# Kernel optimization log

Measured on AMD Instinct MI355X. Metric: run time of the kernel, lower is better.

Reference implementation:

```python
import jax, jax.numpy as jnp
import numpy as np

N_NODES = 50000
D_IN = 128
HIDDEN = 128
UNITS_DENSE = 256
N_EDGES = 600000
N_PRED = 200000
N_SEL = 300000


def setup_inputs() -> dict:
    key = jax.random.key(0)
    ks = jax.random.split(key, 12)
    node_state = jax.random.normal(ks[0], (N_NODES, D_IN), jnp.float32)
    edge_index = jax.random.randint(ks[1], (2, N_EDGES), 0, N_NODES, jnp.int32)
    out_edges = jax.random.randint(ks[2], (2, N_PRED), 0, N_NODES, jnp.int32)
    set_idx = jnp.sort(jax.random.randint(ks[3], (N_SEL,), 0, 2 * N_PRED, jnp.int32))
    # Glorot-ish scaled weights
    W1 = jax.random.normal(ks[4], (D_IN, HIDDEN), jnp.float32) / np.float32(np.sqrt(D_IN))
    b1 = jnp.zeros((HIDDEN,), jnp.float32)
    W2 = jax.random.normal(ks[5], (HIDDEN, HIDDEN), jnp.float32) / np.float32(np.sqrt(HIDDEN))
    b2 = jnp.zeros((HIDDEN,), jnp.float32)
    dense_W = jax.random.normal(ks[6], (2 * 0 + HIDDEN, UNITS_DENSE), jnp.float32) / np.float32(np.sqrt(HIDDEN))
    dense_b = jnp.zeros((UNITS_DENSE,), jnp.float32)
    out_W = jax.random.normal(ks[7], (UNITS_DENSE, 2), jnp.float32) / np.float32(np.sqrt(UNITS_DENSE))
    out_b = jnp.zeros((2,), jnp.float32)
    return {
        "node_state": node_state, "edge_index": edge_index, "out_edges": out_edges,
        "set_idx": set_idx, "W1": W1, "b1": b1, "W2": W2, "b2": b2,
        "dense_W": dense_W, "dense_b": dense_b, "out_W": out_W, "out_b": out_b,
    }


def _graph_conv(h, src, dst, W, b):
    """DGL GraphConv, norm='both', no activation: D_in^{-1/2} A D_out^{-1/2} H W + b."""
    n = h.shape[0]
    ones = jnp.ones(src.shape[0], h.dtype)
    deg_out = jnp.clip(jax.ops.segment_sum(ones, src, num_segments=n), 1.0)  # [N]
    deg_in = jnp.clip(jax.ops.segment_sum(ones, dst, num_segments=n), 1.0)   # [N]
    h = (h * jax.lax.rsqrt(deg_out)[:, None]) @ W                            # [N, H]
    agg = jax.ops.segment_sum(h[src], dst, num_segments=n)                   # [N, H]
    return agg * jax.lax.rsqrt(deg_in)[:, None] + b


def reference(node_state, edge_index, out_edges, set_idx,
              W1, b1, W2, b2, dense_W, dense_b, out_W, out_b):
    src, dst = edge_index[0], edge_index[1]
    h = _graph_conv(node_state, src, dst, W1, b1)
    h = _graph_conv(h, src, dst, W2, b2)
    # concat along axis=0 as in the original: [2*E_pred, H]
    edge_state = jnp.concatenate([h[out_edges[0]], h[out_edges[1]]], axis=0)
    # boolean_mask replaced by equivalent gather of selected (True) rows
    edge_state_set = edge_state[set_idx]                                      # [N_SEL, H]
    hidden = jax.nn.relu(edge_state_set @ dense_W + dense_b)
    return jax.nn.softmax(hidden @ out_W + out_b, axis=-1)
```

## Files before the change

kernel.cpp:

```cpp
#include <hip/hip_runtime.h>

#define NN 50000
#define DD 128
#define NE 600000
#define NP 200000
#define NS 300000
#define NU 256
#define NBH 128
#define EPB 4688
#define NW 12500
#define NB64 782
#define NSCAN 49

typedef __attribute__((ext_vector_type(8))) short short8;
typedef __attribute__((ext_vector_type(4))) float floatx4;

__device__ inline float bf2f(unsigned int u16) {
    unsigned int x = u16 << 16;
    float f; __builtin_memcpy(&f, &x, 4); return f;
}
__device__ inline unsigned short f2bf(float f) {
    unsigned int x; __builtin_memcpy(&x, &f, 4);
    unsigned int lsb = (x >> 16) & 1u;
    x += 0x7fffu + lsb;
    return (unsigned short)(x >> 16);
}

__global__ __launch_bounds__(256) void k_hist(const int* __restrict__ ei,
                                              unsigned int* __restrict__ P,
                                              unsigned long long* __restrict__ status) {
    __shared__ unsigned int hw[NW];
    int b = blockIdx.x, half = blockIdx.y, tid = threadIdx.x;
    if (b == 0 && half == 0 && tid < 64) status[tid] = 0ull;
    for (int w = tid; w < NW; w += 256) hw[w] = 0;
    __syncthreads();
    const int* src = ei + (size_t)half * NE;
    int e0 = b * EPB, e1 = min(e0 + EPB, NE);
    for (int e = e0 + tid; e < e1; e += 256) {
        int s = src[e];
        atomicAdd(&hw[s >> 2], 1u << ((s & 3) * 8));
    }
    __syncthreads();
    unsigned int* Pb = P + ((size_t)half * NBH + b) * NW;
    for (int w = tid; w < NW; w += 256) Pb[w] = hw[w];
}

__global__ __launch_bounds__(256) void k_mid(
    const unsigned int* __restrict__ P_hist, float* __restrict__ r,
    const float* __restrict__ W1, const float* __restrict__ W2, const float* __restrict__ dW,
    unsigned short* __restrict__ BT1, unsigned short* __restrict__ BT2,
    unsigned short* __restrict__ BTd,
    int* __restrict__ row_ptr, unsigned char* __restrict__ baseb,
    unsigned long long* __restrict__ status)
{
    int b = blockIdx.x, tid = threadIdx.x, lane = tid & 63, w = tid >> 6;
    int gid = b * 256 + tid;

    int4 v = {0, 0, 0, 0};
    if (gid < NW) {
        const unsigned int* Ph = P_hist + (size_t)NBH * NW + gid;
        int c0 = 0, c1 = 0, c2 = 0, c3 = 0;
        for (int b2 = 0; b2 < NBH; ++b2) {
            unsigned int x = Ph[(size_t)b2 * NW];
            c0 += x & 0xff; c1 += (x >> 8) & 0xff; c2 += (x >> 16) & 0xff; c3 += x >> 24;
        }
        v = (int4){c0, c1, c2, c3};
        float4 rr = {rsqrtf((float)max(c0, 1)), rsqrtf((float)max(c1, 1)),
                     rsqrtf((float)max(c2, 1)), rsqrtf((float)max(c3, 1))};
        *(float4*)(r + NN + gid * 4) = rr;
    } else if (gid < 2 * NW) {
        int wl = gid - NW;
        const unsigned int* Ph = P_hist + wl;
        int c0 = 0, c1 = 0, c2 = 0, c3 = 0;
        for (int b2 = 0; b2 < NBH; ++b2) {
            unsigned int x = Ph[(size_t)b2 * NW];
            c0 += x & 0xff; c1 += (x >> 8) & 0xff; c2 += (x >> 16) & 0xff; c3 += x >> 24;
        }
        float4 rr = {rsqrtf((float)max(c0, 1)), rsqrtf((float)max(c1, 1)),
                     rsqrtf((float)max(c2, 1)), rsqrtf((float)max(c3, 1))};
        *(float4*)(r + wl * 4) = rr;
    }

    {
        int t = gid;
        if (t < 16384) { int rr = t >> 7, cc = t & 127; BT1[cc * 128 + rr] = f2bf(W1[t]); }
        else if (t < 32768) { int t2 = t - 16384; int rr = t2 >> 7, cc = t2 & 127; BT2[cc * 128 + rr] = f2bf(W2[t2]); }
        else if (t < 65536) { int t2 = t - 32768; int rr = t2 >> 8, cc = t2 & 255; BTd[cc * 128 + rr] = f2bf(dW[t2]); }
    }

    if (b < NSCAN) {
        __shared__ int wsum[4];
        __shared__ long long sbase;
        int tot = v.x + v.y + v.z + v.w;
        int x = tot;
#pragma unroll
        for (int off = 1; off < 64; off <<= 1) {
            int y = __shfl_up(x, off);
            if (lane >= off) x += y;
        }
        if (lane == 63) wsum[w] = x;
        __syncthreads();
        int woff = 0;
#pragma unroll
        for (int i = 0; i < 4; ++i) if (i < w) woff += wsum[i];
        if (tid == 0) {
            int btot = wsum[0] + wsum[1] + wsum[2] + wsum[3];
            if (b == 0) {
                sbase = 0;
                __threadfence();
                atomicExch(&status[0], (2ull << 62) | (unsigned long long)btot);
            } else {
                __threadfence();
                atomicExch(&status[b], (1ull << 62) | (unsigned long long)btot);
                long long run = 0; int j = b - 1;
                while (true) {
                    unsigned long long s;
                    do { s = atomicAdd(&status[j], 0ull); } while (s == 0ull);
                    run += (long long)(s & 0x3fffffffffffffffull);
                    if ((s >> 62) == 2ull) break;
                    --j;
                }
                sbase = run;
                __threadfence();
                atomicExch(&status[b], (2ull << 62) | (unsigned long long)(run + btot));
            }
        }
        __syncthreads();
        if (gid < NW) {
            int base = (int)sbase + woff + (x - tot);
            int4 o = {base, base + v.x, base + v.x + v.y, base + v.x + v.y + v.z};
            *(int4*)(row_ptr + gid * 4) = o;
        }
        if (b == 0 && tid == 0) row_ptr[NN] = NE;
    }

    int cb = b - NSCAN;
    if (cb >= 0 && cb < 196) {
        int n = cb * 256 + tid;
        if (n < NN) {
            int wl = n >> 2, sh = (n & 3) * 8;
            int run = 0;
            const unsigned int* Pd = P_hist + (size_t)NBH * NW;
            for (int b2 = 0; b2 < NBH; ++b2) {
                baseb[(size_t)b2 * NN + n] = (unsigned char)run;
                run += (Pd[(size_t)b2 * NW + wl] >> sh) & 0xff;
            }
        }
    }
}

__global__ __launch_bounds__(256) void k_gemm1_bucket(
    const float* __restrict__ A, const float* __restrict__ rs,
    const unsigned short* __restrict__ BT, unsigned short* __restrict__ Cm,
    const int* __restrict__ ei, const int* __restrict__ row_ptr,
    const unsigned char* __restrict__ baseb, int* __restrict__ col)
{
    __shared__ unsigned short sm[26112];
    int b = blockIdx.x, tid = threadIdx.x;

    if (b < NBH) {
        unsigned int* cw = (unsigned int*)sm;
        for (int w = tid; w < NW; w += 256) cw[w] = 0;
        __syncthreads();
        const unsigned char* bt = baseb + (size_t)b * NN;
        int e0 = b * EPB, e1 = min(e0 + EPB, NE);
        for (int e = e0 + tid; e < e1; e += 256) {
            int s = ei[e], d = ei[NE + e];
            int sh = (d & 3) * 8;
            unsigned int old = atomicAdd(&cw[d >> 2], 1u << sh);
            col[row_ptr[d] + (int)bt[d] + ((old >> sh) & 0xff)] = s;
        }
        return;
    }

    unsigned short (*As)[136] = (unsigned short(*)[136])sm;
    unsigned short (*Bs)[136] = (unsigned short(*)[136])(sm + 64 * 136);
    int lane = tid & 63, wave = tid >> 6;
    int quad = lane >> 4, l16 = lane & 15;
    int row0 = (b - NBH) * 64;

#pragma unroll
    for (int p = 0; p < 8; ++p) {
        int fid = tid + p * 256;
        int r = fid >> 5, c = fid & 31;
        int gr = row0 + r; if (gr > NN - 1) gr = NN - 1;
        float4 v = *(const float4*)(A + (size_t)gr * DD + c * 4);
        ushort4 u;
        u.x = f2bf(v.x); u.y = f2bf(v.y); u.z = f2bf(v.z); u.w = f2bf(v.w);
        *(ushort4*)&As[r][c * 4] = u;
    }
#pragma unroll
    for (int p = 0; p < 8; ++p) {
        int fid = tid + p * 256;
        int r = fid >> 4, c = fid & 15;
        *(uint4*)&Bs[r][c * 8] = *(const uint4*)(BT + (size_t)r * DD + c * 8);
    }
    __syncthreads();

    short8 af[4];
#pragma unroll
    for (int ks = 0; ks < 4; ++ks)
        af[ks] = *(const short8*)&As[wave * 16 + l16][ks * 32 + quad * 8];
    floatx4 acc[8];
#pragma unroll
    for (int nt = 0; nt < 8; ++nt) acc[nt] = (floatx4){0.f, 0.f, 0.f, 0.f};
#pragma unroll
    for (int ks = 0; ks < 4; ++ks) {
#pragma unroll
        for (int nt = 0; nt < 8; ++nt) {
            short8 bf = *(const short8*)&Bs[nt * 16 + l16][ks * 32 + quad * 8];
            acc[nt] = __builtin_amdgcn_mfma_f32_16x16x32_bf16(af[ks], bf, acc[nt], 0, 0, 0);
        }
    }
    int rbase = row0 + wave * 16 + quad * 4;
#pragma unroll
    for (int r = 0; r < 4; ++r) {
        int gr = rbase + r;
        if (gr < NN) {
            float s = rs[gr];
#pragma unroll
            for (int nt = 0; nt < 8; ++nt)
                Cm[(size_t)gr * DD + nt * 16 + l16] = f2bf(acc[nt][r] * s);
        }
    }
}

__global__ __launch_bounds__(256) void k_gemm_bf(const unsigned short* __restrict__ A,
                                                 const float* __restrict__ rs,
                                                 const unsigned short* __restrict__ BT,
                                                 unsigned short* __restrict__ Cm) {
    __shared__ unsigned short As[64][136];
    __shared__ unsigned short Bs[128][136];
    int tid = threadIdx.x, lane = tid & 63, wave = tid >> 6;
    int quad = lane >> 4, l16 = lane & 15;
    int row0 = blockIdx.x * 64;

#pragma unroll
    for (int p = 0; p < 4; ++p) {
        int fid = tid + p * 256;
        int r = fid >> 4, c = fid & 15;
        int gr = row0 + r; if (gr > NN - 1) gr = NN - 1;
        *(uint4*)&As[r][c * 8] = *(const uint4*)(A + (size_t)gr * DD + c * 8);
    }
#pragma unroll
    for (int p = 0; p < 8; ++p) {
        int fid = tid + p * 256;
        int r = fid >> 4, c = fid & 15;
        *(uint4*)&Bs[r][c * 8] = *(const uint4*)(BT + (size_t)r * DD + c * 8);
    }
    __syncthreads();

    short8 af[4];
#pragma unroll
    for (int ks = 0; ks < 4; ++ks)
        af[ks] = *(const short8*)&As[wave * 16 + l16][ks * 32 + quad * 8];
    floatx4 acc[8];
#pragma unroll
    for (int nt = 0; nt < 8; ++nt) acc[nt] = (floatx4){0.f, 0.f, 0.f, 0.f};
#pragma unroll
    for (int ks = 0; ks < 4; ++ks) {
#pragma unroll
        for (int nt = 0; nt < 8; ++nt) {
            short8 bf = *(const short8*)&Bs[nt * 16 + l16][ks * 32 + quad * 8];
            acc[nt] = __builtin_amdgcn_mfma_f32_16x16x32_bf16(af[ks], bf, acc[nt], 0, 0, 0);
        }
    }
    int rbase = row0 + wave * 16 + quad * 4;
#pragma unroll
    for (int r = 0; r < 4; ++r) {
        int gr = rbase + r;
        if (gr < NN) {
            float s = rs[gr];
#pragma unroll
            for (int nt = 0; nt < 8; ++nt)
                Cm[(size_t)gr * DD + nt * 16 + l16] = f2bf(acc[nt][r] * s);
        }
    }
}

__global__ __launch_bounds__(256) void k_aggregate(const unsigned short* __restrict__ T,
                                                   const int* __restrict__ row_ptr,
                                                   const int* __restrict__ col,
                                                   const float* __restrict__ r_in,
                                                   const float* __restrict__ b,
                                                   unsigned short* __restrict__ H) {
    int wave = threadIdx.x >> 6, lane = threadIdx.x & 63;
    int sub = lane >> 4, l16 = lane & 15;
    int node = blockIdx.x * 16 + wave * 4 + sub;
    if (node >= NN) return;
    int beg = row_ptr[node], end = row_ptr[node + 1];
    float a0 = 0.f, a1 = 0.f, a2 = 0.f, a3 = 0.f, a4 = 0.f, a5 = 0.f, a6 = 0.f, a7 = 0.f;
    for (int base = beg; base < end; base += 16) {
        int m = end - base; if (m > 16) m = 16;
        int myidx = (l16 < m) ? col[base + l16] : 0;
        int j = 0;
        for (; j + 4 <= m; j += 4) {
            int s0 = __shfl(myidx, (sub << 4) | j);
            int s1 = __shfl(myidx, (sub << 4) | (j + 1));
            int s2 = __shfl(myidx, (sub << 4) | (j + 2));
            int s3 = __shfl(myidx, (sub << 4) | (j + 3));
            uint4 v0 = *(const uint4*)(T + (size_t)s0 * DD + l16 * 8);
            uint4 v1 = *(const uint4*)(T + (size_t)s1 * DD + l16 * 8);
            uint4 v2 = *(const uint4*)(T + (size_t)s2 * DD + l16 * 8);
            uint4 v3 = *(const uint4*)(T + (size_t)s3 * DD + l16 * 8);
            a0 += bf2f(v0.x & 0xffff) + bf2f(v1.x & 0xffff) + bf2f(v2.x & 0xffff) + bf2f(v3.x & 0xffff);
            a1 += bf2f(v0.x >> 16)    + bf2f(v1.x >> 16)    + bf2f(v2.x >> 16)    + bf2f(v3.x >> 16);
            a2 += bf2f(v0.y & 0xffff) + bf2f(v1.y & 0xffff) + bf2f(v2.y & 0xffff) + bf2f(v3.y & 0xffff);
            a3 += bf2f(v0.y >> 16)    + bf2f(v1.y >> 16)    + bf2f(v2.y >> 16)    + bf2f(v3.y >> 16);
            a4 += bf2f(v0.z & 0xffff) + bf2f(v1.z & 0xffff) + bf2f(v2.z & 0xffff) + bf2f(v3.z & 0xffff);
            a5 += bf2f(v0.z >> 16)    + bf2f(v1.z >> 16)    + bf2f(v2.z >> 16)    + bf2f(v3.z >> 16);
            a6 += bf2f(v0.w & 0xffff) + bf2f(v1.w & 0xffff) + bf2f(v2.w & 0xffff) + bf2f(v3.w & 0xffff);
            a7 += bf2f(v0.w >> 16)    + bf2f(v1.w >> 16)    + bf2f(v2.w >> 16)    + bf2f(v3.w >> 16);
        }
        for (; j < m; ++j) {
            int s0 = __shfl(myidx, (sub << 4) | j);
            uint4 v0 = *(const uint4*)(T + (size_t)s0 * DD + l16 * 8);
            a0 += bf2f(v0.x & 0xffff); a1 += bf2f(v0.x >> 16);
            a2 += bf2f(v0.y & 0xffff); a3 += bf2f(v0.y >> 16);
            a4 += bf2f(v0.z & 0xffff); a5 += bf2f(v0.z >> 16);
            a6 += bf2f(v0.w & 0xffff); a7 += bf2f(v0.w >> 16);
        }
    }
    float rv = r_in[node];
    float4 bl = *(const float4*)(b + l16 * 8);
    float4 bh = *(const float4*)(b + l16 * 8 + 4);
    uint4 w;
    w.x = (unsigned int)f2bf(a0 * rv + bl.x) | ((unsigned int)f2bf(a1 * rv + bl.y) << 16);
    w.y = (unsigned int)f2bf(a2 * rv + bl.z) | ((unsigned int)f2bf(a3 * rv + bl.w) << 16);
    w.z = (unsigned int)f2bf(a4 * rv + bh.x) | ((unsigned int)f2bf(a5 * rv + bh.y) << 16);
    w.w = (unsigned int)f2bf(a6 * rv + bh.z) | ((unsigned int)f2bf(a7 * rv + bh.w) << 16);
    *(uint4*)(H + (size_t)node * DD + l16 * 8) = w;
}

__global__ __launch_bounds__(256) void k_mlp_mfma(const unsigned short* __restrict__ H2,
                                                  const unsigned short* __restrict__ BTd,
                                                  const float* __restrict__ db,
                                                  const float* __restrict__ oW,
                                                  const float* __restrict__ ob,
                                                  float* __restrict__ P) {
    __shared__ unsigned short As[64][136];
    __shared__ unsigned short Bs[128][136];
    int tid = threadIdx.x, lane = tid & 63, wave = tid >> 6;
    int quad = lane >> 4, l16 = lane & 15;
    int row0 = blockIdx.x * 64;
#pragma unroll
    for (int p = 0; p < 4; ++p) {
        int fid = tid + p * 256;
        int r = fid >> 4, c = fid & 15;
        int gr = row0 + r; if (gr > NN - 1) gr = NN - 1;
        *(uint4*)&As[r][c * 8] = *(const uint4*)(H2 + (size_t)gr * DD + c * 8);
    }
    short8 af[4];
    floatx4 acc[16];
#pragma unroll
    for (int i = 0; i < 16; ++i) acc[i] = (floatx4){0.f, 0.f, 0.f, 0.f};

    for (int ch = 0; ch < 2; ++ch) {
        __syncthreads();
#pragma unroll
        for (int p = 0; p < 8; ++p) {
            int fid = tid + p * 256;
            int r = fid >> 4, c = fid & 15;
            *(uint4*)&Bs[r][c * 8] = *(const uint4*)(BTd + (size_t)(ch * 128 + r) * DD + c * 8);
        }
        __syncthreads();
        if (ch == 0) {
#pragma unroll
            for (int ks = 0; ks < 4; ++ks)
                af[ks] = *(const short8*)&As[wave * 16 + l16][ks * 32 + quad * 8];
        }
#pragma unroll
        for (int ks = 0; ks < 4; ++ks) {
#pragma unroll
            for (int nt = 0; nt < 8; ++nt) {
                short8 bf = *(const short8*)&Bs[nt * 16 + l16][ks * 32 + quad * 8];
                acc[ch * 8 + nt] =
                    __builtin_amdgcn_mfma_f32_16x16x32_bf16(af[ks], bf, acc[ch * 8 + nt], 0, 0, 0);
            }
        }
    }
    int rbase = row0 + wave * 16 + quad * 4;
#pragma unroll
    for (int r = 0; r < 4; ++r) {
        float p0 = 0.f, p1 = 0.f;
#pragma unroll
        for (int ch = 0; ch < 2; ++ch) {
#pragma unroll
            for (int nt = 0; nt < 8; ++nt) {
                int colc = ch * 128 + nt * 16 + l16;
                float h = acc[ch * 8 + nt][r] + db[colc];
                h = fmaxf(h, 0.f);
                p0 += h * oW[2 * colc];
                p1 += h * oW[2 * colc + 1];
            }
        }
#pragma unroll
        for (int m = 8; m >= 1; m >>= 1) {
            p0 += __shfl_xor(p0, m, 16);
            p1 += __shfl_xor(p1, m, 16);
        }
        if (l16 == 0) {
            int gr = rbase + r;
            if (gr < NN) {
                float l0 = p0 + ob[0], l1 = p1 + ob[1];
                float mx = fmaxf(l0, l1);
                float e0 = __expf(l0 - mx), e1 = __expf(l1 - mx);
                float inv = 1.f / (e0 + e1);
                float2 pr = {e0 * inv, e1 * inv};
                *(float2*)(P + 2 * gr) = pr;
            }
        }
    }
}

__global__ void k_gather(const int* __restrict__ sidx, const int* __restrict__ oe,
                         const float* __restrict__ P, float* __restrict__ out) {
    int i = blockIdx.x * 256 + threadIdx.x;
    if (i >= NS) return;
    int node = oe[sidx[i]];
    float2 v = *(const float2*)(P + 2 * node);
    *(float2*)(out + 2 * i) = v;
}

extern "C" void kernel_launch(void* const* d_in, const int* in_sizes, int n_in,
                              void* d_out, int out_size, void* d_ws, size_t ws_size,
                              hipStream_t stream) {
    const float* node_state = (const float*)d_in[0];
    const int* ei   = (const int*)d_in[1];
    const int* oe   = (const int*)d_in[2];
    const int* sidx = (const int*)d_in[3];
    const float* W1 = (const float*)d_in[4];
    const float* b1 = (const float*)d_in[5];
    const float* W2 = (const float*)d_in[6];
    const float* b2 = (const float*)d_in[7];
    const float* dW = (const float*)d_in[8];
    const float* db = (const float*)d_in[9];
    const float* oW = (const float*)d_in[10];
    const float* ob = (const float*)d_in[11];
    float* out = (float*)d_out;

    char* ws = (char*)d_ws;
    size_t off = 0;
    auto carve = [&](size_t bytes) -> char* {
        char* p = ws + off;
        off = (off + bytes + 255) & ~(size_t)255;
        return p;
    };
    float* r       = (float*)carve((size_t)2 * NN * 4);
    int*   row_ptr = (int*)carve((size_t)(NN + 1) * 4);
    int*   col     = (int*)carve((size_t)NE * 4);
    unsigned int* P_hist = (unsigned int*)carve((size_t)2 * NBH * NW * 4);
    unsigned char* baseb = (unsigned char*)carve((size_t)NBH * NN);
    unsigned long long* status = (unsigned long long*)carve(64 * 8);
    unsigned short* t   = (unsigned short*)carve((size_t)NN * DD * 2);
    unsigned short* h   = (unsigned short*)carve((size_t)NN * DD * 2);
    unsigned short* BT1 = (unsigned short*)carve((size_t)DD * DD * 2);
    unsigned short* BT2 = (unsigned short*)carve((size_t)DD * DD * 2);
    unsigned short* BTd = (unsigned short*)carve((size_t)DD * NU * 2);
    float* P = (float*)t;

    float* r_out = r;
    float* r_in  = r + NN;

    k_hist<<<dim3(NBH, 2), 256, 0, stream>>>(ei, P_hist, status);
    k_mid<<<256, 256, 0, stream>>>(P_hist, r, W1, W2, dW, BT1, BT2, BTd,
                                   row_ptr, baseb, status);

    k_gemm1_bucket<<<NBH + NB64, 256, 0, stream>>>(node_state, r_out, BT1, t,
                                                   ei, row_ptr, baseb, col);
    k_aggregate<<<(NN + 15) / 16, 256, 0, stream>>>(t, row_ptr, col, r_in, b1, h);

    k_gemm_bf<<<NB64, 256, 0, stream>>>(h, r_out, BT2, t);
    k_aggregate<<<(NN + 15) / 16, 256, 0, stream>>>(t, row_ptr, col, r_in, b2, h);

    k_mlp_mfma<<<NB64, 256, 0, stream>>>(h, BTd, db, oW, ob, P);
    k_gather<<<(NS + 255) / 256, 256, 0, stream>>>(sidx, oe, P, out);
}
```

Baseline: 229.8 us.

## Fuse neighbor aggregation into the following GEMM and MLP kernels

Each aggregation pass now writes its 64-row tile of aggregated features straight into shared memory, and the next MFMA GEMM (layer-2 transform or dense MLP) runs on it in the same block. This removes two kernel launches and the global write and re-read of the intermediate h buffer. In exchange, each block does 64 irregular gather rows before its GEMM, with fewer blocks (782 instead of 3125) and no overlap between the gather-bound and compute phases. The t and h buffers swap roles, and the second layer now writes into h.

```diff
diff --git a/kernel.cpp b/kernel.cpp
--- a/kernel.cpp
+++ b/kernel.cpp
@@ -225,70 +225,14 @@
     }
 }
 
-__global__ __launch_bounds__(256) void k_gemm_bf(const unsigned short* __restrict__ A,
-                                                 const float* __restrict__ rs,
-                                                 const unsigned short* __restrict__ BT,
-                                                 unsigned short* __restrict__ Cm) {
-    __shared__ unsigned short As[64][136];
-    __shared__ unsigned short Bs[128][136];
-    int tid = threadIdx.x, lane = tid & 63, wave = tid >> 6;
-    int quad = lane >> 4, l16 = lane & 15;
-    int row0 = blockIdx.x * 64;
-
-#pragma unroll
-    for (int p = 0; p < 4; ++p) {
-        int fid = tid + p * 256;
-        int r = fid >> 4, c = fid & 15;
-        int gr = row0 + r; if (gr > NN - 1) gr = NN - 1;
-        *(uint4*)&As[r][c * 8] = *(const uint4*)(A + (size_t)gr * DD + c * 8);
-    }
-#pragma unroll
-    for (int p = 0; p < 8; ++p) {
-        int fid = tid + p * 256;
-        int r = fid >> 4, c = fid & 15;
-        *(uint4*)&Bs[r][c * 8] = *(const uint4*)(BT + (size_t)r * DD + c * 8);
-    }
-    __syncthreads();
-
-    short8 af[4];
-#pragma unroll
-    for (int ks = 0; ks < 4; ++ks)
-        af[ks] = *(const short8*)&As[wave * 16 + l16][ks * 32 + quad * 8];
-    floatx4 acc[8];
-#pragma unroll
-    for (int nt = 0; nt < 8; ++nt) acc[nt] = (floatx4){0.f, 0.f, 0.f, 0.f};
-#pragma unroll
-    for (int ks = 0; ks < 4; ++ks) {
-#pragma unroll
-        for (int nt = 0; nt < 8; ++nt) {
-            short8 bf = *(const short8*)&Bs[nt * 16 + l16][ks * 32 + quad * 8];
-            acc[nt] = __builtin_amdgcn_mfma_f32_16x16x32_bf16(af[ks], bf, acc[nt], 0, 0, 0);
-        }
-    }
-    int rbase = row0 + wave * 16 + quad * 4;
-#pragma unroll
-    for (int r = 0; r < 4; ++r) {
-        int gr = rbase + r;
-        if (gr < NN) {
-            float s = rs[gr];
-#pragma unroll
-            for (int nt = 0; nt < 8; ++nt)
-                Cm[(size_t)gr * DD + nt * 16 + l16] = f2bf(acc[nt][r] * s);
-        }
-    }
-}
-
-__global__ __launch_bounds__(256) void k_aggregate(const unsigned short* __restrict__ T,
-                                                   const int* __restrict__ row_ptr,
-                                                   const int* __restrict__ col,
-                                                   const float* __restrict__ r_in,
-                                                   const float* __restrict__ b,
-                                                   unsigned short* __restrict__ H) {
-    int wave = threadIdx.x >> 6, lane = threadIdx.x & 63;
-    int sub = lane >> 4, l16 = lane & 15;
-    int node = blockIdx.x * 16 + wave * 4 + sub;
-    if (node >= NN) return;
-    int beg = row_ptr[node], end = row_ptr[node + 1];
+__device__ inline uint4 agg_row(const unsigned short* __restrict__ T,
+                                const int* __restrict__ row_ptr,
+                                const int* __restrict__ col,
+                                const float* __restrict__ r_in,
+                                const float* __restrict__ bia,
+                                int node, int sub, int l16) {
+    int beg = 0, end = 0;
+    if (node < NN) { beg = row_ptr[node]; end = row_ptr[node + 1]; }
     float a0 = 0.f, a1 = 0.f, a2 = 0.f, a3 = 0.f, a4 = 0.f, a5 = 0.f, a6 = 0.f, a7 = 0.f;
     for (int base = beg; base < end; base += 16) {
         int m = end - base; if (m > 16) m = 16;
@@ -321,35 +265,91 @@
             a6 += bf2f(v0.w & 0xffff); a7 += bf2f(v0.w >> 16);
         }
     }
-    float rv = r_in[node];
-    float4 bl = *(const float4*)(b + l16 * 8);
-    float4 bh = *(const float4*)(b + l16 * 8 + 4);
+    float rv = (node < NN) ? r_in[node] : 0.f;
+    float4 bl = *(const float4*)(bia + l16 * 8);
+    float4 bh = *(const float4*)(bia + l16 * 8 + 4);
     uint4 w;
     w.x = (unsigned int)f2bf(a0 * rv + bl.x) | ((unsigned int)f2bf(a1 * rv + bl.y) << 16);
     w.y = (unsigned int)f2bf(a2 * rv + bl.z) | ((unsigned int)f2bf(a3 * rv + bl.w) << 16);
     w.z = (unsigned int)f2bf(a4 * rv + bh.x) | ((unsigned int)f2bf(a5 * rv + bh.y) << 16);
     w.w = (unsigned int)f2bf(a6 * rv + bh.z) | ((unsigned int)f2bf(a7 * rv + bh.w) << 16);
-    *(uint4*)(H + (size_t)node * DD + l16 * 8) = w;
-}
-
-__global__ __launch_bounds__(256) void k_mlp_mfma(const unsigned short* __restrict__ H2,
-                                                  const unsigned short* __restrict__ BTd,
-                                                  const float* __restrict__ db,
-                                                  const float* __restrict__ oW,
-                                                  const float* __restrict__ ob,
-                                                  float* __restrict__ P) {
+    return w;
+}
+
+__global__ __launch_bounds__(256) void k_agg_gemm(
+    const unsigned short* __restrict__ T,
+    const int* __restrict__ row_ptr, const int* __restrict__ col,
+    const float* __restrict__ r_in, const float* __restrict__ bia,
+    const unsigned short* __restrict__ BT, const float* __restrict__ rs,
+    unsigned short* __restrict__ Cm)
+{
     __shared__ unsigned short As[64][136];
     __shared__ unsigned short Bs[128][136];
     int tid = threadIdx.x, lane = tid & 63, wave = tid >> 6;
-    int quad = lane >> 4, l16 = lane & 15;
+    int sub = lane >> 4, l16 = lane & 15;
     int row0 = blockIdx.x * 64;
-#pragma unroll
-    for (int p = 0; p < 4; ++p) {
+
+    for (int g = 0; g < 4; ++g) {
+        int r = wave * 16 + g * 4 + sub;
+        uint4 w = agg_row(T, row_ptr, col, r_in, bia, row0 + r, sub, l16);
+        *(uint4*)&As[r][l16 * 8] = w;
+    }
+#pragma unroll
+    for (int p = 0; p < 8; ++p) {
         int fid = tid + p * 256;
-        int r = fid >> 4, c = fid & 15;
-        int gr = row0 + r; if (gr > NN - 1) gr = NN - 1;
-        *(uint4*)&As[r][c * 8] = *(const uint4*)(H2 + (size_t)gr * DD + c * 8);
-    }
+        int rr = fid >> 4, c = fid & 15;
+        *(uint4*)&Bs[rr][c * 8] = *(const uint4*)(BT + (size_t)rr * DD + c * 8);
+    }
+    __syncthreads();
+
+    short8 af[4];
+#pragma unroll
+    for (int ks = 0; ks < 4; ++ks)
+        af[ks] = *(const short8*)&As[wave * 16 + l16][ks * 32 + sub * 8];
+    floatx4 acc[8];
+#pragma unroll
+    for (int nt = 0; nt < 8; ++nt) acc[nt] = (floatx4){0.f, 0.f, 0.f, 0.f};
+#pragma unroll
+    for (int ks = 0; ks < 4; ++ks) {
+#pragma unroll
+        for (int nt = 0; nt < 8; ++nt) {
+            short8 bf = *(const short8*)&Bs[nt * 16 + l16][ks * 32 + sub * 8];
+            acc[nt] = __builtin_amdgcn_mfma_f32_16x16x32_bf16(af[ks], bf, acc[nt], 0, 0, 0);
+        }
+    }
+    int rbase = row0 + wave * 16 + sub * 4;
+#pragma unroll
+    for (int r = 0; r < 4; ++r) {
+        int gr = rbase + r;
+        if (gr < NN) {
+            float s = rs[gr];
+#pragma unroll
+            for (int nt = 0; nt < 8; ++nt)
+                Cm[(size_t)gr * DD + nt * 16 + l16] = f2bf(acc[nt][r] * s);
+        }
+    }
+}
+
+__global__ __launch_bounds__(256) void k_agg_mlp(
+    const unsigned short* __restrict__ T,
+    const int* __restrict__ row_ptr, const int* __restrict__ col,
+    const float* __restrict__ r_in, const float* __restrict__ bia,
+    const unsigned short* __restrict__ BTd, const float* __restrict__ db,
+    const float* __restrict__ oW, const float* __restrict__ ob,
+    float* __restrict__ P)
+{
+    __shared__ unsigned short As[64][136];
+    __shared__ unsigned short Bs[128][136];
+    int tid = threadIdx.x, lane = tid & 63, wave = tid >> 6;
+    int sub = lane >> 4, l16 = lane & 15;
+    int row0 = blockIdx.x * 64;
+
+    for (int g = 0; g < 4; ++g) {
+        int r = wave * 16 + g * 4 + sub;
+        uint4 w = agg_row(T, row_ptr, col, r_in, bia, row0 + r, sub, l16);
+        *(uint4*)&As[r][l16 * 8] = w;
+    }
+
     short8 af[4];
     floatx4 acc[16];
 #pragma unroll
@@ -360,26 +360,26 @@
 #pragma unroll
         for (int p = 0; p < 8; ++p) {
             int fid = tid + p * 256;
-            int r = fid >> 4, c = fid & 15;
-            *(uint4*)&Bs[r][c * 8] = *(const uint4*)(BTd + (size_t)(ch * 128 + r) * DD + c * 8);
+            int rr = fid >> 4, c = fid & 15;
+            *(uint4*)&Bs[rr][c * 8] = *(const uint4*)(BTd + (size_t)(ch * 128 + rr) * DD + c * 8);
         }
         __syncthreads();
         if (ch == 0) {
 #pragma unroll
             for (int ks = 0; ks < 4; ++ks)
-                af[ks] = *(const short8*)&As[wave * 16 + l16][ks * 32 + quad * 8];
+                af[ks] = *(const short8*)&As[wave * 16 + l16][ks * 32 + sub * 8];
         }
 #pragma unroll
         for (int ks = 0; ks < 4; ++ks) {
 #pragma unroll
             for (int nt = 0; nt < 8; ++nt) {
-                short8 bf = *(const short8*)&Bs[nt * 16 + l16][ks * 32 + quad * 8];
+                short8 bf = *(const short8*)&Bs[nt * 16 + l16][ks * 32 + sub * 8];
                 acc[ch * 8 + nt] =
                     __builtin_amdgcn_mfma_f32_16x16x32_bf16(af[ks], bf, acc[ch * 8 + nt], 0, 0, 0);
             }
         }
     }
-    int rbase = row0 + wave * 16 + quad * 4;
+    int rbase = row0 + wave * 16 + sub * 4;
 #pragma unroll
     for (int r = 0; r < 4; ++r) {
         float p0 = 0.f, p1 = 0.f;
@@ -468,11 +468,10 @@
 
     k_gemm1_bucket<<<NBH + NB64, 256, 0, stream>>>(node_state, r_out, BT1, t,
                                                    ei, row_ptr, baseb, col);
-    k_aggregate<<<(NN + 15) / 16, 256, 0, stream>>>(t, row_ptr, col, r_in, b1, h);
-
-    k_gemm_bf<<<NB64, 256, 0, stream>>>(h, r_out, BT2, t);
-    k_aggregate<<<(NN + 15) / 16, 256, 0, stream>>>(t, row_ptr, col, r_in, b2, h);
-
-    k_mlp_mfma<<<NB64, 256, 0, stream>>>(h, BTd, db, oW, ob, P);
+
+    k_agg_gemm<<<NB64, 256, 0, stream>>>(t, row_ptr, col, r_in, b1, BT2, r_out, h);
+
+    k_agg_mlp<<<NB64, 256, 0, stream>>>(h, row_ptr, col, r_in, b2, BTd, db, oW, ob, P);
+
     k_gather<<<(NS + 255) / 256, 256, 0, stream>>>(sidx, oe, P, out);
 }
```

After: 247.5 us. 7.7% more time.

## Replace decoupled look-back scan with parallel wavefront reduction, move weight transpose to histogram

Applied to the files above, without the earlier changes.

The histogram kernel now runs 512 threads per block and also converts and transposes the three weight matrices to bf16, so that work leaves the scan kernel. In the scan, the serial chained look-back over the status flags is replaced: each block publishes only its local total, and one wavefront reads all predecessor totals in parallel and reduces them with shuffles. This removes the serial dependency chain across the 49 scan blocks, at the cost of every block spinning on up to 48 flags. The scan grid is trimmed to 245 blocks to match the work that remains.

```diff
diff --git a/kernel.cpp b/kernel.cpp
--- a/kernel.cpp
+++ b/kernel.cpp
@@ -26,30 +26,39 @@
     return (unsigned short)(x >> 16);
 }
 
-__global__ __launch_bounds__(256) void k_hist(const int* __restrict__ ei,
+__global__ __launch_bounds__(512) void k_hist(const int* __restrict__ ei,
                                               unsigned int* __restrict__ P,
-                                              unsigned long long* __restrict__ status) {
+                                              unsigned long long* __restrict__ status,
+                                              const float* __restrict__ W1,
+                                              const float* __restrict__ W2,
+                                              const float* __restrict__ dW,
+                                              unsigned short* __restrict__ BT1,
+                                              unsigned short* __restrict__ BT2,
+                                              unsigned short* __restrict__ BTd) {
     __shared__ unsigned int hw[NW];
     int b = blockIdx.x, half = blockIdx.y, tid = threadIdx.x;
     if (b == 0 && half == 0 && tid < 64) status[tid] = 0ull;
-    for (int w = tid; w < NW; w += 256) hw[w] = 0;
+    for (int w = tid; w < NW; w += 512) hw[w] = 0;
+    {
+        int gid = (half * NBH + b) * 512 + tid;
+        if (gid < 16384) { int rr = gid >> 7, cc = gid & 127; BT1[cc * 128 + rr] = f2bf(W1[gid]); }
+        else if (gid < 32768) { int t2 = gid - 16384; int rr = t2 >> 7, cc = t2 & 127; BT2[cc * 128 + rr] = f2bf(W2[t2]); }
+        else if (gid < 65536) { int t2 = gid - 32768; int rr = t2 >> 8, cc = t2 & 255; BTd[cc * 128 + rr] = f2bf(dW[t2]); }
+    }
     __syncthreads();
     const int* src = ei + (size_t)half * NE;
     int e0 = b * EPB, e1 = min(e0 + EPB, NE);
-    for (int e = e0 + tid; e < e1; e += 256) {
+    for (int e = e0 + tid; e < e1; e += 512) {
         int s = src[e];
         atomicAdd(&hw[s >> 2], 1u << ((s & 3) * 8));
     }
     __syncthreads();
     unsigned int* Pb = P + ((size_t)half * NBH + b) * NW;
-    for (int w = tid; w < NW; w += 256) Pb[w] = hw[w];
+    for (int w = tid; w < NW; w += 512) Pb[w] = hw[w];
 }
 
 __global__ __launch_bounds__(256) void k_mid(
     const unsigned int* __restrict__ P_hist, float* __restrict__ r,
-    const float* __restrict__ W1, const float* __restrict__ W2, const float* __restrict__ dW,
-    unsigned short* __restrict__ BT1, unsigned short* __restrict__ BT2,
-    unsigned short* __restrict__ BTd,
     int* __restrict__ row_ptr, unsigned char* __restrict__ baseb,
     unsigned long long* __restrict__ status)
 {
@@ -81,13 +90,6 @@
         *(float4*)(r + wl * 4) = rr;
     }
 
-    {
-        int t = gid;
-        if (t < 16384) { int rr = t >> 7, cc = t & 127; BT1[cc * 128 + rr] = f2bf(W1[t]); }
-        else if (t < 32768) { int t2 = t - 16384; int rr = t2 >> 7, cc = t2 & 127; BT2[cc * 128 + rr] = f2bf(W2[t2]); }
-        else if (t < 65536) { int t2 = t - 32768; int rr = t2 >> 8, cc = t2 & 255; BTd[cc * 128 + rr] = f2bf(dW[t2]); }
-    }
-
     if (b < NSCAN) {
         __shared__ int wsum[4];
         __shared__ long long sbase;
@@ -103,27 +105,21 @@
         int woff = 0;
 #pragma unroll
         for (int i = 0; i < 4; ++i) if (i < w) woff += wsum[i];
-        if (tid == 0) {
+        if (w == 0) {
             int btot = wsum[0] + wsum[1] + wsum[2] + wsum[3];
-            if (b == 0) {
-                sbase = 0;
-                __threadfence();
-                atomicExch(&status[0], (2ull << 62) | (unsigned long long)btot);
-            } else {
+            if (lane == 0) {
                 __threadfence();
                 atomicExch(&status[b], (1ull << 62) | (unsigned long long)btot);
-                long long run = 0; int j = b - 1;
-                while (true) {
-                    unsigned long long s;
-                    do { s = atomicAdd(&status[j], 0ull); } while (s == 0ull);
-                    run += (long long)(s & 0x3fffffffffffffffull);
-                    if ((s >> 62) == 2ull) break;
-                    --j;
-                }
-                sbase = run;
-                __threadfence();
-                atomicExch(&status[b], (2ull << 62) | (unsigned long long)(run + btot));
-            }
+            }
+            long long run = 0;
+            if (lane < b) {
+                unsigned long long s;
+                do { s = atomicAdd(&status[lane], 0ull); } while (s == 0ull);
+                run = (long long)(s & 0x3fffffffffffffffull);
+            }
+#pragma unroll
+            for (int off = 32; off > 0; off >>= 1) run += __shfl_down(run, off);
+            if (lane == 0) sbase = run;
         }
         __syncthreads();
         if (gid < NW) {
@@ -462,9 +458,9 @@
     float* r_out = r;
     float* r_in  = r + NN;
 
-    k_hist<<<dim3(NBH, 2), 256, 0, stream>>>(ei, P_hist, status);
-    k_mid<<<256, 256, 0, stream>>>(P_hist, r, W1, W2, dW, BT1, BT2, BTd,
-                                   row_ptr, baseb, status);
+    k_hist<<<dim3(NBH, 2), 512, 0, stream>>>(ei, P_hist, status, W1, W2, dW,
+                                             BT1, BT2, BTd);
+    k_mid<<<245, 256, 0, stream>>>(P_hist, r, row_ptr, baseb, status);
 
     k_gemm1_bucket<<<NBH + NB64, 256, 0, stream>>>(node_state, r_out, BT1, t,
                                                    ei, row_ptr, baseb, col);
```

New measurement: 230.8 us. No clear change (+0.4%).
